# Kernel optimization log

Hardware: AMD Instinct MI355X
Metric: run time of the kernel (lower is better)

The kernel has to match this reference:

```python
import jax, jax.numpy as jnp
import numpy as np


def _pairwise_dist(pred, gt):
    # pred: [B, N, 3], gt: [B, M, 3] -> Euclidean distances [B, N, M]
    p2 = jnp.sum(pred * pred, axis=-1)  # [B, N]
    g2 = jnp.sum(gt * gt, axis=-1)      # [B, M]
    cross = jnp.einsum('bnd,bmd->bnm', pred, gt)  # [B, N, M]
    d2 = p2[:, :, None] + g2[:, None, :] - 2.0 * cross
    return jnp.sqrt(jnp.maximum(d2, 1e-12))


def setup_inputs() -> dict:
    key = jax.random.key(0)
    k1, k2 = jax.random.split(key)
    pred = jax.random.normal(k1, (32, 4096, 3), dtype=jnp.float32)
    gt = jax.random.normal(k2, (32, 4096, 3), dtype=jnp.float32)
    return {"pred": pred, "gt": gt}


def reference(pred, gt):
    dist = _pairwise_dist(pred, gt)              # [B, N, M]
    chamfer1 = jnp.mean(jnp.min(dist, axis=1))   # min over pred points (dim=1)
    chamfer2 = jnp.mean(jnp.min(dist, axis=2))   # min over gt points (dim=2)
    return chamfer1 + chamfer2
```

## Files before the change

### kernel.cpp

```cpp
#include <hip/hip_runtime.h>
#include <math.h>


typedef short short8 __attribute__((ext_vector_type(8)));
typedef float f32x16 __attribute__((ext_vector_type(16)));
typedef unsigned int uint;

#define NPTS  4096
#define TPBM  512
#define TPBP  256
#define GRID_MAIN 1024
#define CHT   32
#define NCH   2
#define NROWS (2 * 32 * NPTS)
#define ONEB ((short)0x3F80)

__device__ __forceinline__ unsigned short bf16h(float f) {
    uint u = __float_as_uint(f);
    uint r = u + 0x7FFFu + ((u >> 16) & 1u);
    return (unsigned short)(r >> 16);
}
__device__ __forceinline__ float bf16f(unsigned short h) {
    return __uint_as_float(((uint)h) << 16);
}
struct Split2 { unsigned short h, m; };
__device__ __forceinline__ Split2 split2(float x) {
    Split2 s;
    s.h = bf16h(x);
    s.m = bf16h(x - bf16f(s.h));
    return s;
}

__global__ __launch_bounds__(TPBM, 4) void chamfer_mfma(
    const float* __restrict__ pred,
    const float* __restrict__ gt,
    float* __restrict__ wsrow)
{
    const int bx    = blockIdx.x;
    const int dir   = bx >> 9;
    const int rem   = bx & 511;
    const int b     = rem >> 4;
    const int sub   = rem & 15;
    const int panel = sub >> 1;
    const int thalf = sub & 1;
    const int tid   = threadIdx.x;
    const int lane  = tid & 63, wid = tid >> 6;
    const int c31   = lane & 31, half = lane >> 5;

    __shared__ short8 sB[CHT * 64];

    const float* qsrc = (dir ? pred : gt) + (size_t)b * NPTS * 3;
    const float* tsrc = (dir ? gt : pred) + (size_t)b * NPTS * 3;

    short8 afr[2];
    float gm[2][16];
#pragma unroll
    for (int fr = 0; fr < 2; ++fr) {
        const int row = panel * 512 + wid * 64 + fr * 32 + c31;
        const float* ap = qsrc + (size_t)row * 3;
        float x = ap[0], y = ap[1], z = ap[2];
        Split2 X = split2(-2.0f*x), Y = split2(-2.0f*y), Z = split2(-2.0f*z);
        Split2 Q2 = split2(fmaf(x, x, fmaf(y, y, z * z)));
        short8 a;
        if (half == 0) {
            a[0]=(short)X.h; a[1]=(short)Y.h; a[2]=(short)Z.h;
            a[3]=(short)X.h; a[4]=(short)Y.h; a[5]=(short)Z.h;
            a[6]=(short)X.m; a[7]=(short)Y.m;
        } else {
            a[0]=(short)Z.m; a[1]=(short)X.m; a[2]=(short)Y.m; a[3]=(short)Z.m;
            a[4]=(short)Q2.h; a[5]=(short)Q2.m; a[6]=ONEB; a[7]=ONEB;
        }
        afr[fr] = a;
#pragma unroll
        for (int r = 0; r < 16; ++r) gm[fr][r] = 1e30f;
    }

    const f32x16 zero = {0.f,0.f,0.f,0.f,0.f,0.f,0.f,0.f,
                         0.f,0.f,0.f,0.f,0.f,0.f,0.f,0.f};

    const int tbase = thalf * (NCH * CHT);
    float rx[4], ry[4], rz[4];
#pragma unroll
    for (int ps = 0; ps < 4; ++ps) {
        const int u  = ps * TPBM + tid;
        const int pt = (tbase + (u >> 6)) * 32 + (u & 31);
        const float* p = tsrc + (size_t)pt * 3;
        rx[ps] = p[0]; ry[ps] = p[1]; rz[ps] = p[2];
    }

    for (int ch = 0; ch < NCH; ++ch) {
        __syncthreads();
#pragma unroll
        for (int ps = 0; ps < 4; ++ps) {
            const int u = ps * TPBM + tid;
            float x = rx[ps], y = ry[ps], z = rz[ps];
            Split2 X = split2(x), Y = split2(y), Z = split2(z);
            short8 f;
            if (((u >> 5) & 1) == 0) {
                f[0]=(short)X.h; f[1]=(short)Y.h; f[2]=(short)Z.h;
                f[3]=(short)X.m; f[4]=(short)Y.m; f[5]=(short)Z.m;
                f[6]=(short)X.h; f[7]=(short)Y.h;
            } else {
                Split2 T2 = split2(fmaf(x, x, fmaf(y, y, z * z)));
                f[0]=(short)Z.h; f[1]=(short)X.m; f[2]=(short)Y.m;
                f[3]=(short)Z.m; f[4]=ONEB; f[5]=ONEB;
                f[6]=(short)T2.h; f[7]=(short)T2.m;
            }
            sB[u] = f;
        }
        __syncthreads();

        const int chn = (ch + 1 < NCH) ? ch + 1 : ch;
#pragma unroll
        for (int ps = 0; ps < 4; ++ps) {
            const int u  = ps * TPBM + tid;
            const int pt = (tbase + chn * CHT + (u >> 6)) * 32 + (u & 31);
            const float* p = tsrc + (size_t)pt * 3;
            rx[ps] = p[0]; ry[ps] = p[1]; rz[ps] = p[2];
        }

#pragma unroll 4
        for (int t = 0; t < CHT; ++t) {
            short8 bfr = sB[t * 64 + lane];
            f32x16 a0 = __builtin_amdgcn_mfma_f32_32x32x16_bf16(
                afr[0], bfr, zero, 0, 0, 0);
            f32x16 a1 = __builtin_amdgcn_mfma_f32_32x32x16_bf16(
                afr[1], bfr, zero, 0, 0, 0);
#pragma unroll
            for (int r = 0; r < 16; ++r) {
                gm[0][r] = fminf(gm[0][r], a0[r]);
                gm[1][r] = fminf(gm[1][r], a1[r]);
            }
        }
    }

#pragma unroll
    for (int off = 1; off < 32; off <<= 1)
#pragma unroll
        for (int fr = 0; fr < 2; ++fr)
#pragma unroll
            for (int r = 0; r < 16; ++r)
                gm[fr][r] = fminf(gm[fr][r], __shfl_xor(gm[fr][r], off, 64));

    if (c31 == 0) {
        const int rowbase = (dir * 32 + b) * NPTS + panel * 512 + wid * 64;
        float* w = wsrow + (size_t)thalf * NROWS + rowbase;
#pragma unroll
        for (int fr = 0; fr < 2; ++fr)
#pragma unroll
            for (int r = 0; r < 16; ++r)
                w[fr * 32 + (r & 3) + 8 * (r >> 2) + 4 * half] = gm[fr][r];
    }
}

__global__ __launch_bounds__(TPBP) void chamfer_finish(
    const float* __restrict__ wsrow, float* __restrict__ out)
{
    __shared__ float swv[TPBP / 64];
    const int tid  = threadIdx.x;
    const int base = blockIdx.x * (TPBP * 8) + tid;

    float s = 0.0f;
#pragma unroll
    for (int r = 0; r < 8; ++r) {
        const int i = base + r * TPBP;
        float v = fminf(wsrow[i], wsrow[NROWS + i]);
        s += sqrtf(fmaxf(v, 1e-12f));
    }

#pragma unroll
    for (int off = 32; off > 0; off >>= 1) s += __shfl_down(s, off, 64);
    const int wid = tid >> 6, lane = tid & 63;
    if (lane == 0) swv[wid] = s;
    __syncthreads();
    if (tid == 0) {
        float tot = swv[0] + swv[1] + swv[2] + swv[3];
        atomicAdd(out, tot * (1.0f / 131072.0f));
    }
}

extern "C" void kernel_launch(void* const* d_in, const int* in_sizes, int n_in,
                              void* d_out, int out_size, void* d_ws, size_t ws_size,
                              hipStream_t stream)
{
    const float* pred = (const float*)d_in[0];
    const float* gt   = (const float*)d_in[1];
    float* out        = (float*)d_out;
    float* wsrow      = (float*)d_ws;

    hipMemsetAsync(d_out, 0, sizeof(float), stream);

    chamfer_mfma<<<dim3(GRID_MAIN), dim3(TPBM), 0, stream>>>(pred, gt, wsrow);
    chamfer_finish<<<dim3(NROWS / (TPBP * 8)), dim3(TPBP), 0, stream>>>(
        wsrow, out);
}
```

Before: 102.8 us.

## Compute both chamfer directions from a single distance tile pass

Instead of computing the distance matrix twice (once per direction), each block now computes gt-vs-pred tiles once and derives both row minima (per gt point, in registers) and column minima (per pred point, via shared-memory atomicMin on float bits). Per-panel column minima are written to workspace and reduced across 16 panels in the finish kernel. This halves the MFMA work but adds per-iteration cross-lane min reduction and LDS atomics, plus a larger workspace and extra finish-kernel reads.

```diff
diff --git a/kernel.cpp b/kernel.cpp
--- a/kernel.cpp
+++ b/kernel.cpp
@@ -9,10 +9,10 @@
 #define NPTS  4096
 #define TPBM  512
 #define TPBP  256
-#define GRID_MAIN 1024
-#define CHT   32
-#define NCH   2
-#define NROWS (2 * 32 * NPTS)
+#define NPANEL 16
+#define GRID_MAIN (32 * NPANEL)
+#define CHT   16
+#define NCH   4
 #define ONEB ((short)0x3F80)
 
 __device__ __forceinline__ unsigned short bf16h(float f) {
@@ -34,33 +34,36 @@
 __global__ __launch_bounds__(TPBM, 4) void chamfer_mfma(
     const float* __restrict__ pred,
     const float* __restrict__ gt,
-    float* __restrict__ wsrow)
+    float* __restrict__ wsgt,
+    float* __restrict__ wspp)
 {
     const int bx    = blockIdx.x;
-    const int dir   = bx >> 9;
-    const int rem   = bx & 511;
-    const int b     = rem >> 4;
-    const int sub   = rem & 15;
-    const int panel = sub >> 1;
-    const int thalf = sub & 1;
+    const int b     = bx >> 4;
+    const int panel = bx & 15;
     const int tid   = threadIdx.x;
     const int lane  = tid & 63, wid = tid >> 6;
+    const int rw    = wid >> 1;
+    const int cq    = wid & 1;
     const int c31   = lane & 31, half = lane >> 5;
 
-    __shared__ short8 sB[CHT * 64];
-
-    const float* qsrc = (dir ? pred : gt) + (size_t)b * NPTS * 3;
-    const float* tsrc = (dir ? gt : pred) + (size_t)b * NPTS * 3;
+    __shared__ short8 sB[2 * CHT * 64];
+    __shared__ uint   sPmin[NPTS];
+    __shared__ float  sred[256 * 2];
+
+    const float* qsrc = gt   + (size_t)b * NPTS * 3;
+    const float* tsrc = pred + (size_t)b * NPTS * 3;
+
+    for (int c = tid; c < NPTS; c += TPBM) sPmin[c] = 0x7F7FFFFFu;
 
     short8 afr[2];
     float gm[2][16];
 #pragma unroll
     for (int fr = 0; fr < 2; ++fr) {
-        const int row = panel * 512 + wid * 64 + fr * 32 + c31;
+        const int row = panel * 256 + rw * 64 + fr * 32 + c31;
         const float* ap = qsrc + (size_t)row * 3;
         float x = ap[0], y = ap[1], z = ap[2];
         Split2 X = split2(-2.0f*x), Y = split2(-2.0f*y), Z = split2(-2.0f*z);
-        Split2 Q2 = split2(fmaf(x, x, fmaf(y, y, z * z)));
+        Split2 G2 = split2(fmaf(x, x, fmaf(y, y, z * z)));
         short8 a;
         if (half == 0) {
             a[0]=(short)X.h; a[1]=(short)Y.h; a[2]=(short)Z.h;
@@ -68,7 +71,7 @@
             a[6]=(short)X.m; a[7]=(short)Y.m;
         } else {
             a[0]=(short)Z.m; a[1]=(short)X.m; a[2]=(short)Y.m; a[3]=(short)Z.m;
-            a[4]=(short)Q2.h; a[5]=(short)Q2.m; a[6]=ONEB; a[7]=ONEB;
+            a[4]=(short)G2.h; a[5]=(short)G2.m; a[6]=ONEB; a[7]=ONEB;
         }
         afr[fr] = a;
 #pragma unroll
@@ -78,12 +81,11 @@
     const f32x16 zero = {0.f,0.f,0.f,0.f,0.f,0.f,0.f,0.f,
                          0.f,0.f,0.f,0.f,0.f,0.f,0.f,0.f};
 
-    const int tbase = thalf * (NCH * CHT);
     float rx[4], ry[4], rz[4];
 #pragma unroll
     for (int ps = 0; ps < 4; ++ps) {
         const int u  = ps * TPBM + tid;
-        const int pt = (tbase + (u >> 6)) * 32 + (u & 31);
+        const int pt = (((u >> 10) * 64) + ((u >> 6) & 15)) * 32 + (u & 31);
         const float* p = tsrc + (size_t)pt * 3;
         rx[ps] = p[0]; ry[ps] = p[1]; rz[ps] = p[2];
     }
@@ -101,10 +103,10 @@
                 f[3]=(short)X.m; f[4]=(short)Y.m; f[5]=(short)Z.m;
                 f[6]=(short)X.h; f[7]=(short)Y.h;
             } else {
-                Split2 T2 = split2(fmaf(x, x, fmaf(y, y, z * z)));
+                Split2 P2 = split2(fmaf(x, x, fmaf(y, y, z * z)));
                 f[0]=(short)Z.h; f[1]=(short)X.m; f[2]=(short)Y.m;
                 f[3]=(short)Z.m; f[4]=ONEB; f[5]=ONEB;
-                f[6]=(short)T2.h; f[7]=(short)T2.m;
+                f[6]=(short)P2.h; f[7]=(short)P2.m;
             }
             sB[u] = f;
         }
@@ -114,25 +116,36 @@
 #pragma unroll
         for (int ps = 0; ps < 4; ++ps) {
             const int u  = ps * TPBM + tid;
-            const int pt = (tbase + chn * CHT + (u >> 6)) * 32 + (u & 31);
+            const int pt = (((u >> 10) * 64) + chn * CHT + ((u >> 6) & 15)) * 32
+                           + (u & 31);
             const float* p = tsrc + (size_t)pt * 3;
             rx[ps] = p[0]; ry[ps] = p[1]; rz[ps] = p[2];
         }
 
 #pragma unroll 4
         for (int t = 0; t < CHT; ++t) {
-            short8 bfr = sB[t * 64 + lane];
+            short8 bfr = sB[(cq * CHT + t) * 64 + lane];
             f32x16 a0 = __builtin_amdgcn_mfma_f32_32x32x16_bf16(
                 afr[0], bfr, zero, 0, 0, 0);
             f32x16 a1 = __builtin_amdgcn_mfma_f32_32x32x16_bf16(
                 afr[1], bfr, zero, 0, 0, 0);
+
+            float tmin = 1e30f;
 #pragma unroll
             for (int r = 0; r < 16; ++r) {
                 gm[0][r] = fminf(gm[0][r], a0[r]);
                 gm[1][r] = fminf(gm[1][r], a1[r]);
+                tmin = fminf(tmin, fminf(a0[r], a1[r]));
             }
-        }
-    }
+            atomicMin(&sPmin[cq * 2048 + (ch * CHT + t) * 32 + c31],
+                      __float_as_uint(fmaxf(tmin, 1e-12f)));
+        }
+    }
+    __syncthreads();
+
+    float* wp = wspp + (size_t)bx * NPTS;
+    for (int c = tid; c < NPTS; c += TPBM)
+        wp[c] = __uint_as_float(sPmin[c]);
 
 #pragma unroll
     for (int off = 1; off < 32; off <<= 1)
@@ -141,31 +154,44 @@
 #pragma unroll
             for (int r = 0; r < 16; ++r)
                 gm[fr][r] = fminf(gm[fr][r], __shfl_xor(gm[fr][r], off, 64));
-
     if (c31 == 0) {
-        const int rowbase = (dir * 32 + b) * NPTS + panel * 512 + wid * 64;
-        float* w = wsrow + (size_t)thalf * NROWS + rowbase;
 #pragma unroll
         for (int fr = 0; fr < 2; ++fr)
 #pragma unroll
             for (int r = 0; r < 16; ++r)
-                w[fr * 32 + (r & 3) + 8 * (r >> 2) + 4 * half] = gm[fr][r];
+                sred[(rw*64 + fr*32 + (r&3) + 8*(r>>2) + 4*half) * 2 + cq]
+                    = gm[fr][r];
+    }
+    __syncthreads();
+
+    if (tid < 256) {
+        float v = fminf(sred[tid * 2], sred[tid * 2 + 1]);
+        wsgt[(size_t)bx * 256 + tid] = v;
     }
 }
 
 __global__ __launch_bounds__(TPBP) void chamfer_finish(
-    const float* __restrict__ wsrow, float* __restrict__ out)
+    const float* __restrict__ wsgt, const float* __restrict__ wspp,
+    float* __restrict__ out)
 {
     __shared__ float swv[TPBP / 64];
-    const int tid  = threadIdx.x;
-    const int base = blockIdx.x * (TPBP * 8) + tid;
-
+    const int tid = threadIdx.x;
     float s = 0.0f;
-#pragma unroll
-    for (int r = 0; r < 8; ++r) {
-        const int i = base + r * TPBP;
-        float v = fminf(wsrow[i], wsrow[NROWS + i]);
+
+#pragma unroll
+    for (int i = 0; i < 4; ++i) {
+        const int slot = blockIdx.x * (TPBP * 4) + i * TPBP + tid;
+        const int b = slot >> 12, c = slot & 4095;
+        const float* base = wspp + ((size_t)b * 16) * NPTS + c;
+        float v = 1e30f;
+#pragma unroll
+        for (int p = 0; p < 16; ++p) v = fminf(v, base[(size_t)p * NPTS]);
         s += sqrtf(fmaxf(v, 1e-12f));
+    }
+#pragma unroll
+    for (int i = 0; i < 4; ++i) {
+        const int idx = blockIdx.x * (TPBP * 4) + i * TPBP + tid;
+        s += sqrtf(fmaxf(wsgt[idx], 1e-12f));
     }
 
 #pragma unroll
@@ -186,11 +212,14 @@
     const float* pred = (const float*)d_in[0];
     const float* gt   = (const float*)d_in[1];
     float* out        = (float*)d_out;
-    float* wsrow      = (float*)d_ws;
+
+    float* wsgt = (float*)d_ws;
+    float* wspp = (float*)((char*)d_ws + (1 << 20));
 
     hipMemsetAsync(d_out, 0, sizeof(float), stream);
 
-    chamfer_mfma<<<dim3(GRID_MAIN), dim3(TPBM), 0, stream>>>(pred, gt, wsrow);
-    chamfer_finish<<<dim3(NROWS / (TPBP * 8)), dim3(TPBP), 0, stream>>>(
-        wsrow, out);
-}
+    chamfer_mfma<<<dim3(GRID_MAIN), dim3(TPBM), 0, stream>>>(
+        pred, gt, wsgt, wspp);
+    chamfer_finish<<<dim3(131072 / (TPBP * 4)), dim3(TPBP), 0, stream>>>(
+        wsgt, wspp, out);
+}
```

Result: slower. 113.6 us (+10.5%).
